# Optimization experiments

Measured on AMD Instinct MI355X. Metric: run time of the kernel, lower is better.

The kernel has to match this reference:

```python
import jax, jax.numpy as jnp
import numpy as np


def _diffuse(x, A):
    # x: [B,C,N,L], A: [B,V,W] -> out[b,c,v,l] = sum_w x[b,c,w,l] * A[b,v,w]
    return jnp.einsum('ncwl,nvw->ncvl', x, A)


def setup_inputs() -> dict:
    key = jax.random.key(0)
    kx, k0, k1, k2, kw = jax.random.split(key, 5)
    B, C, N, L = 32, 40, 512, 12
    C_OUT = 20
    C_CAT = 7 * C  # (order*support_len + 1) * c_in = (2*3+1)*40
    x = jax.random.normal(kx, (B, C, N, L), dtype=jnp.float32)
    def mk_support(k):
        a = jax.random.uniform(k, (B, N, N), dtype=jnp.float32)
        return a / jnp.sum(a, axis=-1, keepdims=True)  # row-normalized transition
    A0, A1, A2 = mk_support(k0), mk_support(k1), mk_support(k2)
    # Conv2d(c_cat, c_out, kernel=(1,2), dilation=2) weights, stored [c_out, c_cat, 2]
    W = jax.random.normal(kw, (C_OUT, C_CAT, 2), dtype=jnp.float32) * 0.05
    b = jnp.zeros((C_OUT,), dtype=jnp.float32)
    return {'x': x, 'A0': A0, 'A1': A1, 'A2': A2, 'W': W, 'b': b}


def reference(x, A0, A1, A2, W, b):
    # dgcn.forward (eval mode, dropout is identity): order=2, support_len=3
    out = [x]
    for A in (A0, A1, A2):
        x1 = _diffuse(x, A)
        out.append(x1)
        x2 = _diffuse(x1, A)
        out.append(x2)
    h = jnp.concatenate(out, axis=1)  # [B, 7C, N, L]
    # linear_: Conv2d kernel (1,2), dilation 2, no padding -> taps at t and t+2, L_out = L-2
    y = (jnp.einsum('ncvl,oc->novl', h[..., :-2], W[:, :, 0])
         + jnp.einsum('ncvl,oc->novl', h[..., 2:], W[:, :, 1])
         + b[None, :, None, None])
    return y
```

## Files before the change

### kernel.cpp

```cpp
#include <hip/hip_runtime.h>
#include <hip/hip_bf16.h>


typedef unsigned short u16;
typedef u16 u16x4 __attribute__((ext_vector_type(4)));
typedef u16 u16x8 __attribute__((ext_vector_type(8)));
typedef __bf16 bf16x8 __attribute__((ext_vector_type(8)));
typedef float f32x4 __attribute__((ext_vector_type(4)));

#define GLD_LDS16(g, l)  __builtin_amdgcn_global_load_lds( \
    (const __attribute__((address_space(1))) void*)(g),    \
    (__attribute__((address_space(3))) void*)(l), 16, 0, 0)

__device__ __forceinline__ u16 f2bf(float f) {
    unsigned int u = __float_as_uint(f);
    u += 0x7fffu + ((u >> 16) & 1u);
    return (u16)(u >> 16);
}
__device__ __forceinline__ float bf2f(u16 h) {
    return __uint_as_float(((unsigned int)h) << 16);
}

__global__ __launch_bounds__(256) void xpose(const float* __restrict__ x,
                                             u16* __restrict__ xq)
{
    const int t = threadIdx.x, vloc = t & 63, cg = t >> 6;
    const int v = blockIdx.x * 64 + vloc, b = blockIdx.y;

    u16 vals[12][12];
    #pragma unroll
    for (int ci = 0; ci < 12; ++ci) {
        int c = cg * 12 + ci;
        if (c < 40) {
            const float* xp = x + ((size_t)(b * 40 + c) * 512 + v) * 12;
            float4 f0 = *(const float4*)xp;
            float4 f1 = *(const float4*)(xp + 4);
            float4 f2 = *(const float4*)(xp + 8);
            vals[0][ci] = f2bf(f0.x);  vals[1][ci] = f2bf(f0.y);
            vals[2][ci] = f2bf(f0.z);  vals[3][ci] = f2bf(f0.w);
            vals[4][ci] = f2bf(f1.x);  vals[5][ci] = f2bf(f1.y);
            vals[6][ci] = f2bf(f1.z);  vals[7][ci] = f2bf(f1.w);
            vals[8][ci] = f2bf(f2.x);  vals[9][ci] = f2bf(f2.y);
            vals[10][ci] = f2bf(f2.z); vals[11][ci] = f2bf(f2.w);
        } else {
            #pragma unroll
            for (int l = 0; l < 12; ++l) vals[l][ci] = 0;
        }
    }
    #pragma unroll
    for (int l = 0; l < 12; ++l) {
        u16* dst = xq + ((size_t)(b * 12 + l) * 512 + v) * 48 + cg * 12;
        u16x4 a = { vals[l][0], vals[l][1], vals[l][2], vals[l][3] };
        u16x4 c4 = { vals[l][4], vals[l][5], vals[l][6], vals[l][7] };
        u16x4 d = { vals[l][8], vals[l][9], vals[l][10], vals[l][11] };
        *(u16x4*)(dst) = a;
        *(u16x4*)(dst + 4) = c4;
        *(u16x4*)(dst + 8) = d;
    }
}

__global__ __launch_bounds__(256) void proj_x(
    const u16* __restrict__ xq, const float* __restrict__ W,
    u16* __restrict__ P1, u16* __restrict__ P2, u16* __restrict__ proj0)
{
    __shared__ u16 sA[144 * 104];
    __shared__ u16 sB[2][2 * 64 * 48];

    const int t = threadIdx.x, lane = t & 63, wid = t >> 6;
    const int b = blockIdx.y, v0 = blockIdx.x * 64;

    for (int id = t; id < 144 * 5; id += 256) {
        int m = id / 5, c0 = (id % 5) * 8;
        u16x8 e = {}, o8 = {};
        if (m < 140) {
            int o = m % 20, sg = m / 20;
            const float* wp = W + o * 560 + sg * 80 + c0 * 2;
            float4 a = *(const float4*)wp;
            float4 bb = *(const float4*)(wp + 4);
            float4 c = *(const float4*)(wp + 8);
            float4 d = *(const float4*)(wp + 12);
            e[0] = f2bf(a.x);  o8[0] = f2bf(a.y);  e[1] = f2bf(a.z);  o8[1] = f2bf(a.w);
            e[2] = f2bf(bb.x); o8[2] = f2bf(bb.y); e[3] = f2bf(bb.z); o8[3] = f2bf(bb.w);
            e[4] = f2bf(c.x);  o8[4] = f2bf(c.y);  e[5] = f2bf(c.z);  o8[5] = f2bf(c.w);
            e[6] = f2bf(d.x);  o8[6] = f2bf(d.y);  e[7] = f2bf(d.z);  o8[7] = f2bf(d.w);
        }
        *(u16x8*)(&sA[m * 104 + c0]) = e;
        *(u16x8*)(&sA[m * 104 + 40 + c0]) = o8;
    }
    for (int id = t; id < 144 * 3; id += 256) {
        int m = id / 3, k0 = 80 + (id % 3) * 8;
        u16x8 z = {};
        *(u16x8*)(&sA[m * 104 + k0]) = z;
    }

    auto stage = [&](int l, int buf) {
        u16* dst = &sB[buf][0];
        #pragma unroll
        for (int i = 0; i < 3; ++i) {
            int op = wid * 3 + i;
            int tap = op / 6, rem = op % 6;
            const u16* src = xq + ((size_t)(b * 12 + l + 2 * tap) * 512 + v0) * 48
                             + rem * 512 + lane * 8;
            GLD_LDS16(src, dst + tap * 3072 + rem * 512);
        }
    };

    stage(0, 0);
    __syncthreads();

    const int lr = lane & 15, q = lane >> 4;
    bf16x8 af[9][3];
    #pragma unroll
    for (int mf = 0; mf < 9; ++mf)
        #pragma unroll
        for (int s = 0; s < 3; ++s)
            af[mf][s] = *(const bf16x8*)(&sA[(mf * 16 + lr) * 104 + s * 32 + q * 8]);

    const int voff = (wid * 16 + lr) * 48;
    int boff[3];
    #pragma unroll
    for (int s = 0; s < 3; ++s) {
        int k = s * 32 + q * 8;
        int tap, c;
        if (k < 40)      { tap = 0; c = k; }
        else if (k < 80) { tap = 1; c = k - 40; }
        else             { tap = 1; c = 40; }
        boff[s] = tap * 3072 + voff + c;
    }

    const int v = v0 + wid * 16 + lr;
    for (int l = 0; l < 10; ++l) {
        const int cur = l & 1;
        if (l < 9) stage(l + 1, cur ^ 1);

        const u16* bb = &sB[cur][0];
        bf16x8 xf[3];
        #pragma unroll
        for (int s = 0; s < 3; ++s) xf[s] = *(const bf16x8*)(bb + boff[s]);

        f32x4 acc[9] = {};
        #pragma unroll
        for (int s = 0; s < 3; ++s)
            #pragma unroll
            for (int mf = 0; mf < 9; ++mf)
                acc[mf] = __builtin_amdgcn_mfma_f32_16x16x32_bf16(
                    af[mf][s], xf[s], acc[mf], 0, 0, 0);

        #pragma unroll
        for (int mf = 0; mf < 9; ++mf)
            #pragma unroll
            for (int i = 0; i < 4; ++i) {
                int m = mf * 16 + q * 4 + i;
                if (m < 140) {
                    int o = m % 20, sg = m / 20;
                    float val = acc[mf][i];
                    if (sg == 0) {
                        proj0[((size_t)(b * 20 + o) * 10 + l) * 512 + v] = f2bf(val);
                    } else {
                        int s2 = (sg - 1) >> 1;
                        u16* dst = ((sg - 1) & 1) ? P2 : P1;
                        dst[((size_t)(s2 * 32 + b) * 200 + o * 10 + l) * 512 + v] = f2bf(val);
                    }
                }
            }
        __syncthreads();
    }
}

template <int EPI>
__device__ __forceinline__ void gemm_body(
    const float* __restrict__ A0, const float* __restrict__ A1, const float* __restrict__ A2,
    const u16* __restrict__ Xsrc, u16* __restrict__ Odst)
{
    __shared__ char smem[61440];
    float* sAf = (float*)smem;
    u16*   sXs = (u16*)(smem + 32768);

    const int bid = blockIdx.x;
    const int eid = (bid & 7) * 48 + (bid >> 3);
    const int z = eid >> 2;
    const int vblk = (eid & 3) * 128;
    const int s = z >> 5, b = z & 31;

    const float* Af = (s == 0 ? A0 : (s == 1 ? A1 : A2)) + (size_t)b * 512 * 512;
    const u16* Xb = Xsrc + (size_t)z * 200 * 512;

    const int t = threadIdx.x;
    const int lane = t & 63, wid = t >> 6;
    const int lr = lane & 15, q = lane >> 4;
    const int kc0 = q * 2;

    auto stage = [&](int kt, int buf) {
        const int w0 = kt * 32;
        float* ab = sAf + buf * 4096;
        u16*   xb = sXs + buf * 7168;
        #pragma unroll
        for (int i = 0; i < 4; ++i) {
            int op  = wid * 4 + i;
            int row = op * 8 + (lane >> 3);
            int pc  = lane & 7;
            const float* src = Af + (size_t)(vblk + row) * 512 + w0 + ((pc ^ (row & 7)) << 2);
            GLD_LDS16(src, ab + op * 256);
        }
        #pragma unroll
        for (int i = 0; i < 4; ++i) {
            int op = wid + i * 4;
            if (op < 14) {
                int row = op * 16 + (lane >> 2);
                int ch  = lane & 3;
                const u16* src = Xb + (size_t)row * 512 + w0 + ch * 8;
                GLD_LDS16(src, xb + op * 512);
            }
        }
    };

    f32x4 acc[14][2] = {};

    stage(0, 0);
    __syncthreads();

    for (int kt = 0; kt < 16; ++kt) {
        const int cur = kt & 1;
        if (kt < 15) stage(kt + 1, cur ^ 1);

        bf16x8 af[2];
        #pragma unroll
        for (int mf = 0; mf < 2; ++mf) {
            int r = wid * 32 + mf * 16 + lr;
            const float* rb = sAf + cur * 4096 + r * 32;
            f32x4 a0 = *(const f32x4*)(rb + ((kc0 ^ (r & 7)) << 2));
            f32x4 a1 = *(const f32x4*)(rb + (((kc0 + 1) ^ (r & 7)) << 2));
            union { u16x8 u; bf16x8 bv; } cv;
            cv.u = (u16x8){ f2bf(a0[0]), f2bf(a0[1]), f2bf(a0[2]), f2bf(a0[3]),
                            f2bf(a1[0]), f2bf(a1[1]), f2bf(a1[2]), f2bf(a1[3]) };
            af[mf] = cv.bv;
        }
        #pragma unroll
        for (int cf = 0; cf < 14; ++cf) {
            bf16x8 xf = *(const bf16x8*)(sXs + cur * 7168 + (cf * 16 + lr) * 32 + q * 8);
            #pragma unroll
            for (int mf = 0; mf < 2; ++mf)
                acc[cf][mf] = __builtin_amdgcn_mfma_f32_16x16x32_bf16(
                    xf, af[mf], acc[cf][mf], 0, 0, 0);
        }
        __syncthreads();
    }

    u16* eb = (u16*)smem;
    #pragma unroll
    for (int cf = 0; cf < 14; ++cf)
        #pragma unroll
        for (int mf = 0; mf < 2; ++mf)
            #pragma unroll
            for (int i = 0; i < 4; ++i) {
                int col = cf * 16 + q * 4 + i;
                int vl  = wid * 32 + mf * 16 + lr;
                eb[col * 132 + vl] = f2bf(acc[cf][mf][i]);
            }
    __syncthreads();
    u16* Oz = Odst + (size_t)z * 200 * 512;
    for (int id = t; id < 224 * 16; id += 256) {
        int col = id >> 4, ch = id & 15;
        if (col < 200) {
            u16x8 tv = *(const u16x8*)(&eb[col * 132 + ch * 8]);
            size_t gidx = (size_t)col * 512 + vblk + ch * 8;
            if (EPI == 0) {
                u16x8 pv = *(const u16x8*)(Oz + gidx);
                u16x8 out;
                #pragma unroll
                for (int j = 0; j < 8; ++j) out[j] = f2bf(bf2f(tv[j]) + bf2f(pv[j]));
                *(u16x8*)(Oz + gidx) = out;
            } else {
                *(u16x8*)(Oz + gidx) = tv;
            }
        }
    }
}

__global__ __launch_bounds__(256) void gemm_t(
    const float* __restrict__ A0, const float* __restrict__ A1, const float* __restrict__ A2,
    const u16* __restrict__ P2, u16* __restrict__ T)
{
    gemm_body<0>(A0, A1, A2, P2, T);
}

__global__ __launch_bounds__(256) void gemm_yp(
    const float* __restrict__ A0, const float* __restrict__ A1, const float* __restrict__ A2,
    const u16* __restrict__ T, u16* __restrict__ Ypart)
{
    gemm_body<1>(A0, A1, A2, T, Ypart);
}

__global__ __launch_bounds__(256) void reduce_y(
    const u16* __restrict__ Ypart, const u16* __restrict__ proj0,
    const float* __restrict__ bias, float* __restrict__ y)
{
    int i = blockIdx.x * 256 + threadIdx.x;
    if (i >= 32 * 20 * 512) return;
    int v = i & 511;
    int r = i >> 9;
    int o = r % 20, b = r / 20;
    float bb = bias[o];
    float* yp = y + ((size_t)r * 512 + v) * 10;
    #pragma unroll
    for (int l = 0; l < 10; ++l) {
        float sum = bb + bf2f(proj0[((size_t)r * 10 + l) * 512 + v]);
        #pragma unroll
        for (int s = 0; s < 3; ++s)
            sum += bf2f(Ypart[((size_t)(s * 32 + b) * 200 + o * 10 + l) * 512 + v]);
        yp[l] = sum;
    }
}

extern "C" void kernel_launch(void* const* d_in, const int* in_sizes, int n_in,
                              void* d_out, int out_size, void* d_ws, size_t ws_size,
                              hipStream_t stream) {
    const float* x    = (const float*)d_in[0];
    const float* A0   = (const float*)d_in[1];
    const float* A1   = (const float*)d_in[2];
    const float* A2   = (const float*)d_in[3];
    const float* W    = (const float*)d_in[4];
    const float* bias = (const float*)d_in[5];
    float* y = (float*)d_out;

    const size_t PSZ = (size_t)96 * 200 * 512;
    u16* P1 = (u16*)d_ws;
    u16* P2 = P1 + PSZ;
    u16* proj0 = P2 + PSZ;
    u16* Ypart = proj0 + (size_t)32 * 20 * 10 * 512;
    u16* xq = Ypart;

    xpose<<<dim3(8, 32), 256, 0, stream>>>(x, xq);
    proj_x<<<dim3(8, 32), 256, 0, stream>>>(xq, W, P1, P2, proj0);
    gemm_t<<<dim3(384), 256, 0, stream>>>(A0, A1, A2, P2, P1);
    gemm_yp<<<dim3(384), 256, 0, stream>>>(A0, A1, A2, P1, Ypart);
    reduce_y<<<dim3(1280), 256, 0, stream>>>(Ypart, proj0, bias, y);
}
```

Measured before the change: 100.4 us.

## Pre-convert supports to bf16 k-tiled layout once, reuse across both GEMMs

Adds a pass that converts the three fp32 support matrices to bf16 in a k-tile-major layout, once per call. Both diffusion GEMMs then stream half as many bytes of A, and the per-iteration fp32-to-bf16 conversion in the inner loop goes away. The LDS swizzle changes to suit 64-byte bf16 rows. This costs an extra kernel launch plus a full read and write of the converted A, and workspace buffers are re-aliased (Ypart now overlays P2, Abt overlays xq).

New measurement: 125.7 us. +25.2%, slower.

```diff
diff --git a/kernel.cpp b/kernel.cpp
--- a/kernel.cpp
+++ b/kernel.cpp
@@ -167,49 +167,90 @@
     }
 }
 
+__global__ __launch_bounds__(256) void a2bt(
+    const float* __restrict__ A0, const float* __restrict__ A1,
+    const float* __restrict__ A2, u16* __restrict__ Abt)
+{
+    const int vg = blockIdx.x, z = blockIdx.y;
+    const int s = z >> 5, b = z & 31;
+    const float* src = (s == 0 ? A0 : (s == 1 ? A1 : A2))
+                       + (size_t)b * 262144 + (size_t)vg * 64 * 512;
+    const int t = threadIdx.x;
+    const int row = t >> 2, seg = t & 3;
+    const float* p = src + row * 512 + seg * 128;
+    u16* dbase = Abt + (size_t)z * 16 * 16384 + (size_t)(vg * 64 + row) * 32;
+
+    #pragma unroll
+    for (int kc = 0; kc < 4; ++kc) {
+        const float* pp = p + kc * 32;
+        float4 v0 = *(const float4*)(pp);
+        float4 v1 = *(const float4*)(pp + 4);
+        float4 v2 = *(const float4*)(pp + 8);
+        float4 v3 = *(const float4*)(pp + 12);
+        float4 v4 = *(const float4*)(pp + 16);
+        float4 v5 = *(const float4*)(pp + 20);
+        float4 v6 = *(const float4*)(pp + 24);
+        float4 v7 = *(const float4*)(pp + 28);
+        u16x8 o0 = { f2bf(v0.x), f2bf(v0.y), f2bf(v0.z), f2bf(v0.w),
+                     f2bf(v1.x), f2bf(v1.y), f2bf(v1.z), f2bf(v1.w) };
+        u16x8 o1 = { f2bf(v2.x), f2bf(v2.y), f2bf(v2.z), f2bf(v2.w),
+                     f2bf(v3.x), f2bf(v3.y), f2bf(v3.z), f2bf(v3.w) };
+        u16x8 o2 = { f2bf(v4.x), f2bf(v4.y), f2bf(v4.z), f2bf(v4.w),
+                     f2bf(v5.x), f2bf(v5.y), f2bf(v5.z), f2bf(v5.w) };
+        u16x8 o3 = { f2bf(v6.x), f2bf(v6.y), f2bf(v6.z), f2bf(v6.w),
+                     f2bf(v7.x), f2bf(v7.y), f2bf(v7.z), f2bf(v7.w) };
+        const int kt = seg * 4 + kc;
+        u16* d = dbase + (size_t)kt * 16384;
+        *(u16x8*)(d)      = o0;
+        *(u16x8*)(d + 8)  = o1;
+        *(u16x8*)(d + 16) = o2;
+        *(u16x8*)(d + 24) = o3;
+    }
+}
+
+#define SWZ(r) (((r) & 3) ^ (((r) >> 2) & 3))
+
 template <int EPI>
 __device__ __forceinline__ void gemm_body(
-    const float* __restrict__ A0, const float* __restrict__ A1, const float* __restrict__ A2,
+    const u16* __restrict__ Abt,
     const u16* __restrict__ Xsrc, u16* __restrict__ Odst)
 {
-    __shared__ char smem[61440];
-    float* sAf = (float*)smem;
-    u16*   sXs = (u16*)(smem + 32768);
+    __shared__ __align__(16) char smem[59136];
+    u16* sA = (u16*)smem;
+    u16* sX = (u16*)(smem + 16384);
 
     const int bid = blockIdx.x;
     const int eid = (bid & 7) * 48 + (bid >> 3);
     const int z = eid >> 2;
     const int vblk = (eid & 3) * 128;
-    const int s = z >> 5, b = z & 31;
-
-    const float* Af = (s == 0 ? A0 : (s == 1 ? A1 : A2)) + (size_t)b * 512 * 512;
+
+    const u16* Ab = Abt + (size_t)z * 16 * 16384;
     const u16* Xb = Xsrc + (size_t)z * 200 * 512;
 
     const int t = threadIdx.x;
     const int lane = t & 63, wid = t >> 6;
     const int lr = lane & 15, q = lane >> 4;
-    const int kc0 = q * 2;
 
     auto stage = [&](int kt, int buf) {
         const int w0 = kt * 32;
-        float* ab = sAf + buf * 4096;
-        u16*   xb = sXs + buf * 7168;
-        #pragma unroll
-        for (int i = 0; i < 4; ++i) {
-            int op  = wid * 4 + i;
-            int row = op * 8 + (lane >> 3);
-            int pc  = lane & 7;
-            const float* src = Af + (size_t)(vblk + row) * 512 + w0 + ((pc ^ (row & 7)) << 2);
-            GLD_LDS16(src, ab + op * 256);
+        u16* ab = sA + buf * 4096;
+        u16* xb = sX + buf * 7168;
+        const u16* Asrc = Ab + (size_t)kt * 16384 + (size_t)vblk * 32;
+        #pragma unroll
+        for (int i = 0; i < 2; ++i) {
+            int op = wid * 2 + i;
+            int r  = op * 16 + (lane >> 2);
+            int c  = lane & 3;
+            GLD_LDS16(Asrc + r * 32 + ((c ^ SWZ(r)) * 8), ab + op * 512);
         }
         #pragma unroll
         for (int i = 0; i < 4; ++i) {
             int op = wid + i * 4;
             if (op < 14) {
                 int row = op * 16 + (lane >> 2);
-                int ch  = lane & 3;
-                const u16* src = Xb + (size_t)row * 512 + w0 + ch * 8;
-                GLD_LDS16(src, xb + op * 512);
+                int c   = lane & 3;
+                GLD_LDS16(Xb + (size_t)row * 512 + w0 + (c ^ SWZ(row)) * 8,
+                          xb + op * 512);
             }
         }
     };
@@ -227,17 +268,12 @@
         #pragma unroll
         for (int mf = 0; mf < 2; ++mf) {
             int r = wid * 32 + mf * 16 + lr;
-            const float* rb = sAf + cur * 4096 + r * 32;
-            f32x4 a0 = *(const f32x4*)(rb + ((kc0 ^ (r & 7)) << 2));
-            f32x4 a1 = *(const f32x4*)(rb + (((kc0 + 1) ^ (r & 7)) << 2));
-            union { u16x8 u; bf16x8 bv; } cv;
-            cv.u = (u16x8){ f2bf(a0[0]), f2bf(a0[1]), f2bf(a0[2]), f2bf(a0[3]),
-                            f2bf(a1[0]), f2bf(a1[1]), f2bf(a1[2]), f2bf(a1[3]) };
-            af[mf] = cv.bv;
+            af[mf] = *(const bf16x8*)(sA + cur * 4096 + r * 32 + ((q ^ SWZ(r)) * 8));
         }
         #pragma unroll
         for (int cf = 0; cf < 14; ++cf) {
-            bf16x8 xf = *(const bf16x8*)(sXs + cur * 7168 + (cf * 16 + lr) * 32 + q * 8);
+            int rx = cf * 16 + lr;
+            bf16x8 xf = *(const bf16x8*)(sX + cur * 7168 + rx * 32 + ((q ^ SWZ(rx)) * 8));
             #pragma unroll
             for (int mf = 0; mf < 2; ++mf)
                 acc[cf][mf] = __builtin_amdgcn_mfma_f32_16x16x32_bf16(
@@ -278,17 +314,15 @@
 }
 
 __global__ __launch_bounds__(256) void gemm_t(
-    const float* __restrict__ A0, const float* __restrict__ A1, const float* __restrict__ A2,
-    const u16* __restrict__ P2, u16* __restrict__ T)
-{
-    gemm_body<0>(A0, A1, A2, P2, T);
+    const u16* __restrict__ Abt, const u16* __restrict__ P2, u16* __restrict__ T)
+{
+    gemm_body<0>(Abt, P2, T);
 }
 
 __global__ __launch_bounds__(256) void gemm_yp(
-    const float* __restrict__ A0, const float* __restrict__ A1, const float* __restrict__ A2,
-    const u16* __restrict__ T, u16* __restrict__ Ypart)
-{
-    gemm_body<1>(A0, A1, A2, T, Ypart);
+    const u16* __restrict__ Abt, const u16* __restrict__ T, u16* __restrict__ Ypart)
+{
+    gemm_body<1>(Abt, T, Ypart);
 }
 
 __global__ __launch_bounds__(256) void reduce_y(
@@ -327,12 +361,15 @@
     u16* P1 = (u16*)d_ws;
     u16* P2 = P1 + PSZ;
     u16* proj0 = P2 + PSZ;
-    u16* Ypart = proj0 + (size_t)32 * 20 * 10 * 512;
-    u16* xq = Ypart;
+    u16* tail = proj0 + (size_t)32 * 20 * 10 * 512;
+    u16* xq  = tail;
+    u16* Abt = tail;
+    u16* Ypart = P2;
 
     xpose<<<dim3(8, 32), 256, 0, stream>>>(x, xq);
     proj_x<<<dim3(8, 32), 256, 0, stream>>>(xq, W, P1, P2, proj0);
-    gemm_t<<<dim3(384), 256, 0, stream>>>(A0, A1, A2, P2, P1);
-    gemm_yp<<<dim3(384), 256, 0, stream>>>(A0, A1, A2, P1, Ypart);
+    a2bt<<<dim3(8, 96), 256, 0, stream>>>(A0, A1, A2, Abt);
+    gemm_t<<<dim3(384), 256, 0, stream>>>(Abt, P2, P1);
+    gemm_yp<<<dim3(384), 256, 0, stream>>>(Abt, P1, Ypart);
     reduce_y<<<dim3(1280), 256, 0, stream>>>(Ypart, proj0, bias, y);
 }
```

## Preload full A row-block as bf16 in LDS and halve GEMM tile height

Applied to the files above, without the earlier changes.

The GEMM kernels now convert the block's whole 64x512 slice of the fp32 support matrix to bf16 once, upfront into LDS. This replaces streaming fp32 A tiles and converting them in every k-step. The M tile shrinks from 128 to 64 rows, which doubles the grid to 768 blocks. X tiles get an XOR swizzle to avoid LDS bank conflicts. The trade-offs are a 78KB LDS footprint that limits occupancy and the loss of double buffering, so each X load is followed by a sync before compute.

After: 137.8 us. 1.37x slower.

```diff
diff --git a/kernel.cpp b/kernel.cpp
--- a/kernel.cpp
+++ b/kernel.cpp
@@ -11,6 +11,8 @@
 #define GLD_LDS16(g, l)  __builtin_amdgcn_global_load_lds( \
     (const __attribute__((address_space(1))) void*)(g),    \
     (__attribute__((address_space(3))) void*)(l), 16, 0, 0)
+
+#define SWZ(r) (((r) & 3) ^ (((r) >> 2) & 3))
 
 __device__ __forceinline__ u16 f2bf(float f) {
     unsigned int u = __float_as_uint(f);
@@ -172,97 +174,81 @@
     const float* __restrict__ A0, const float* __restrict__ A1, const float* __restrict__ A2,
     const u16* __restrict__ Xsrc, u16* __restrict__ Odst)
 {
-    __shared__ char smem[61440];
-    float* sAf = (float*)smem;
-    u16*   sXs = (u16*)(smem + 32768);
+    __shared__ __align__(16) char smem[79872];
+    u16* sA = (u16*)smem;
+    u16* sX = (u16*)(smem + 65536);
 
     const int bid = blockIdx.x;
-    const int eid = (bid & 7) * 48 + (bid >> 3);
-    const int z = eid >> 2;
-    const int vblk = (eid & 3) * 128;
+    const int eid = (bid & 7) * 96 + (bid >> 3);
+    const int z = eid >> 3, rem = eid & 7;
+    const int vblk = rem * 64;
     const int s = z >> 5, b = z & 31;
 
-    const float* Af = (s == 0 ? A0 : (s == 1 ? A1 : A2)) + (size_t)b * 512 * 512;
-    const u16* Xb = Xsrc + (size_t)z * 200 * 512;
+    const float* Af = (s == 0 ? A0 : (s == 1 ? A1 : A2)) + (size_t)b * 262144;
+    const u16* Xb = Xsrc + (size_t)z * 102400;
 
     const int t = threadIdx.x;
     const int lane = t & 63, wid = t >> 6;
     const int lr = lane & 15, q = lane >> 4;
-    const int kc0 = q * 2;
-
-    auto stage = [&](int kt, int buf) {
+
+    {
+        const float* src = Af + (size_t)vblk * 512;
+        #pragma unroll
+        for (int it = 0; it < 32; ++it) {
+            int g = it * 256 + t;
+            float4 v = *(const float4*)(src + (size_t)g * 4);
+            int row = g >> 7;
+            int k   = (g & 127) * 4;
+            u16x4 pk = { f2bf(v.x), f2bf(v.y), f2bf(v.z), f2bf(v.w) };
+            *(u16x4*)(sA + row * 512 + (((k >> 3) ^ (row & 7)) << 3) + (k & 7)) = pk;
+        }
+    }
+
+    auto stageX = [&](int kt) {
         const int w0 = kt * 32;
-        float* ab = sAf + buf * 4096;
-        u16*   xb = sXs + buf * 7168;
-        #pragma unroll
-        for (int i = 0; i < 4; ++i) {
-            int op  = wid * 4 + i;
-            int row = op * 8 + (lane >> 3);
-            int pc  = lane & 7;
-            const float* src = Af + (size_t)(vblk + row) * 512 + w0 + ((pc ^ (row & 7)) << 2);
-            GLD_LDS16(src, ab + op * 256);
-        }
         #pragma unroll
         for (int i = 0; i < 4; ++i) {
             int op = wid + i * 4;
             if (op < 14) {
                 int row = op * 16 + (lane >> 2);
-                int ch  = lane & 3;
-                const u16* src = Xb + (size_t)row * 512 + w0 + ch * 8;
-                GLD_LDS16(src, xb + op * 512);
+                int c   = lane & 3;
+                GLD_LDS16(Xb + (size_t)row * 512 + w0 + ((c ^ SWZ(row)) * 8),
+                          sX + op * 512);
             }
         }
     };
 
-    f32x4 acc[14][2] = {};
-
-    stage(0, 0);
+    f32x4 acc[14] = {};
+    const int r = wid * 16 + lr;
+
+    for (int kt = 0; kt < 16; ++kt) {
+        stageX(kt);
+        __syncthreads();
+
+        bf16x8 af = *(const bf16x8*)(sA + r * 512 + (((kt * 4 + q) ^ (r & 7)) << 3));
+        #pragma unroll
+        for (int cf = 0; cf < 14; ++cf) {
+            int rx = cf * 16 + lr;
+            bf16x8 xf = *(const bf16x8*)(sX + rx * 32 + ((q ^ SWZ(rx)) * 8));
+            acc[cf] = __builtin_amdgcn_mfma_f32_16x16x32_bf16(xf, af, acc[cf], 0, 0, 0);
+        }
+        __syncthreads();
+    }
+
+    u16* eb = sA;
+    #pragma unroll
+    for (int cf = 0; cf < 14; ++cf)
+        #pragma unroll
+        for (int i = 0; i < 4; ++i) {
+            int col = cf * 16 + q * 4 + i;
+            eb[col * 72 + wid * 16 + lr] = f2bf(acc[cf][i]);
+        }
     __syncthreads();
-
-    for (int kt = 0; kt < 16; ++kt) {
-        const int cur = kt & 1;
-        if (kt < 15) stage(kt + 1, cur ^ 1);
-
-        bf16x8 af[2];
-        #pragma unroll
-        for (int mf = 0; mf < 2; ++mf) {
-            int r = wid * 32 + mf * 16 + lr;
-            const float* rb = sAf + cur * 4096 + r * 32;
-            f32x4 a0 = *(const f32x4*)(rb + ((kc0 ^ (r & 7)) << 2));
-            f32x4 a1 = *(const f32x4*)(rb + (((kc0 + 1) ^ (r & 7)) << 2));
-            union { u16x8 u; bf16x8 bv; } cv;
-            cv.u = (u16x8){ f2bf(a0[0]), f2bf(a0[1]), f2bf(a0[2]), f2bf(a0[3]),
-                            f2bf(a1[0]), f2bf(a1[1]), f2bf(a1[2]), f2bf(a1[3]) };
-            af[mf] = cv.bv;
-        }
-        #pragma unroll
-        for (int cf = 0; cf < 14; ++cf) {
-            bf16x8 xf = *(const bf16x8*)(sXs + cur * 7168 + (cf * 16 + lr) * 32 + q * 8);
-            #pragma unroll
-            for (int mf = 0; mf < 2; ++mf)
-                acc[cf][mf] = __builtin_amdgcn_mfma_f32_16x16x32_bf16(
-                    xf, af[mf], acc[cf][mf], 0, 0, 0);
-        }
-        __syncthreads();
-    }
-
-    u16* eb = (u16*)smem;
-    #pragma unroll
-    for (int cf = 0; cf < 14; ++cf)
-        #pragma unroll
-        for (int mf = 0; mf < 2; ++mf)
-            #pragma unroll
-            for (int i = 0; i < 4; ++i) {
-                int col = cf * 16 + q * 4 + i;
-                int vl  = wid * 32 + mf * 16 + lr;
-                eb[col * 132 + vl] = f2bf(acc[cf][mf][i]);
-            }
-    __syncthreads();
-    u16* Oz = Odst + (size_t)z * 200 * 512;
-    for (int id = t; id < 224 * 16; id += 256) {
-        int col = id >> 4, ch = id & 15;
+    u16* Oz = Odst + (size_t)z * 102400;
+    for (int id = t; id < 224 * 8; id += 256) {
+        int col = id >> 3, ch = id & 7;
         if (col < 200) {
-            u16x8 tv = *(const u16x8*)(&eb[col * 132 + ch * 8]);
+            u16x8 tv = *(const u16x8*)(eb + col * 72 + ch * 8);
             size_t gidx = (size_t)col * 512 + vblk + ch * 8;
             if (EPI == 0) {
                 u16x8 pv = *(const u16x8*)(Oz + gidx);
@@ -332,7 +318,7 @@
 
     xpose<<<dim3(8, 32), 256, 0, stream>>>(x, xq);
     proj_x<<<dim3(8, 32), 256, 0, stream>>>(xq, W, P1, P2, proj0);
-    gemm_t<<<dim3(384), 256, 0, stream>>>(A0, A1, A2, P2, P1);
-    gemm_yp<<<dim3(384), 256, 0, stream>>>(A0, A1, A2, P1, Ypart);
+    gemm_t<<<dim3(768), 256, 0, stream>>>(A0, A1, A2, P2, P1);
+    gemm_yp<<<dim3(768), 256, 0, stream>>>(A0, A1, A2, P1, Ypart);
     reduce_y<<<dim3(1280), 256, 0, stream>>>(Ypart, proj0, bias, y);
 }
```
